# Optimization experiments

Hardware: AMD Instinct MI355X
Metric: run time of the kernel (lower is better)

Reference implementation:

```python
import jax, jax.numpy as jnp
import numpy as np

H = 128
NUM_GRAPHS = 256
NUM_TASKS = 40
BN_EPS = 1e-5


def setup_inputs() -> dict:
    key = jax.random.key(0)
    ks = jax.random.split(key, 32)
    N, E, F = 50000, 600000, 9
    inp = {}
    inp["x"] = jax.random.randint(ks[0], (N, 1), 0, 2)
    inp["edge_index"] = jax.random.randint(ks[1], (2, E), 0, N)
    inp["edge_attr"] = jax.random.uniform(ks[2], (E, F), dtype=jnp.float32)
    inp["batch"] = jnp.sort(jax.random.randint(ks[3], (N,), 0, NUM_GRAPHS))
    inp["self_loop_index"] = 7
    inp["self_loop_type"] = 1
    # parameters
    s = 0.02
    inp["node_emb"] = jax.random.normal(ks[4], (2, H), jnp.float32) * s
    for l in range(2):
        o = 5 + l * 11
        inp[f"enc_w{l}"] = jax.random.normal(ks[o + 0], (F, H), jnp.float32) * s
        inp[f"enc_b{l}"] = jnp.zeros((H,), jnp.float32)
        inp[f"w1_{l}"] = jax.random.normal(ks[o + 1], (2 * H, 2 * H), jnp.float32) * s
        inp[f"b1_{l}"] = jnp.zeros((2 * H,), jnp.float32)
        inp[f"gamma{l}"] = jnp.ones((2 * H,), jnp.float32)
        inp[f"beta{l}"] = jnp.zeros((2 * H,), jnp.float32)
        inp[f"mean{l}"] = jax.random.normal(ks[o + 2], (2 * H,), jnp.float32) * 0.1
        inp[f"var{l}"] = jax.random.uniform(ks[o + 3], (2 * H,), jnp.float32, 0.5, 1.5)
        inp[f"w2_{l}"] = jax.random.normal(ks[o + 4], (2 * H, H), jnp.float32) * s
        inp[f"b2_{l}"] = jnp.zeros((H,), jnp.float32)
    inp["pred_w"] = jax.random.normal(ks[30], (2 * H, NUM_TASKS), jnp.float32) * s
    inp["pred_b"] = jnp.zeros((NUM_TASKS,), jnp.float32)
    return inp


def _gin_layer(h, ei, ea, N, enc_w, enc_b, w1, b1, gamma, beta, mean, var, w2, b2):
    # edge encode: Linear(F, H) on all (real + self-loop) edges
    e = ea @ enc_w + enc_b                                  # [E+N, H]
    msg = jnp.concatenate([h[ei[1]], e], axis=1)            # [E+N, 2H] (feature_concat)
    agg = jax.ops.segment_sum(msg, ei[0], num_segments=N)   # sum pooling -> [N, 2H]
    z = agg @ w1 + b1
    z = (z - mean) * jax.lax.rsqrt(var + BN_EPS) * gamma + beta  # BatchNorm1d (eval)
    z = jax.nn.relu(z)
    return z @ w2 + b2                                      # [N, H]


def reference(x, edge_index, edge_attr, batch, self_loop_index, self_loop_type,
              node_emb,
              enc_w0, enc_b0, w1_0, b1_0, gamma0, beta0, mean0, var0, w2_0, b2_0,
              enc_w1, enc_b1, w1_1, b1_1, gamma1, beta1, mean1, var1, w2_1, b2_1,
              pred_w, pred_b):
    N = x.shape[0]
    loop = jnp.arange(N, dtype=edge_index.dtype)
    ei = jnp.concatenate([edge_index, jnp.stack([loop, loop])], axis=1)  # add self loops
    sl_attr = jnp.zeros((N, edge_attr.shape[1]), edge_attr.dtype).at[:, self_loop_index].set(
        jnp.asarray(self_loop_type, edge_attr.dtype))
    ea = jnp.concatenate([edge_attr, sl_attr], axis=0)       # [E+N, F]

    h0 = node_emb[x.reshape(-1)]                             # input node embedding [N, H]
    h1 = jax.nn.relu(_gin_layer(h0, ei, ea, N, enc_w0, enc_b0, w1_0, b1_0,
                                gamma0, beta0, mean0, var0, w2_0, b2_0))
    h2 = _gin_layer(h1, ei, ea, N, enc_w1, enc_b1, w1_1, b1_1,
                    gamma1, beta1, mean1, var1, w2_1, b2_1)  # JK='last'

    # graph mean pooling over batch ids
    sums = jax.ops.segment_sum(h2, batch, num_segments=NUM_GRAPHS)
    cnt = jax.ops.segment_sum(jnp.ones((N,), h2.dtype), batch, num_segments=NUM_GRAPHS)
    pooled = sums / jnp.maximum(cnt, 1.0)[:, None]
    graph_rep = jnp.concatenate([pooled, pooled], axis=1)    # no center_node_idx
    return graph_rep @ pred_w + pred_b                       # [G, num_tasks]
```

## Files before the change

kernel.cpp:

```cpp
#include <hip/hip_runtime.h>

#define H   128
#define H2  256
#define NG  256
#define NT  40
#define NF  9
#define TBM 32

__global__ void k_h0(const int* __restrict__ x, const float* __restrict__ emb,
                     float* __restrict__ h, int N) {
  int i = blockIdx.x * blockDim.x + threadIdx.x;
  if (i >= N * 32) return;
  int v = i >> 5, q = i & 31;
  ((float4*)h)[i] = ((const float4*)emb)[x[v] * 32 + q];
}

__global__ void k_deg(const int* __restrict__ ei, unsigned* __restrict__ deg, int E) {
  int e = blockIdx.x * blockDim.x + threadIdx.x;
  if (e >= E) return;
  atomicAdd(&deg[ei[e]], 1u);
}

__global__ __launch_bounds__(1024) void k_scan(const unsigned* __restrict__ deg,
                                               unsigned* __restrict__ off,
                                               unsigned* __restrict__ cur, int N) {
  __shared__ unsigned wsum[16];
  __shared__ unsigned wpre[16];
  __shared__ unsigned s_run;
  int tid = threadIdx.x;
  int lane = tid & 63, wv = tid >> 6;
  if (tid == 0) s_run = 0u;
  __syncthreads();
  for (int base = 0; base < N; base += 4096) {
    int i0 = base + tid * 4;
    unsigned v0 = 0, v1 = 0, v2 = 0, v3 = 0;
    if (i0 + 0 < N) v0 = deg[i0 + 0];
    if (i0 + 1 < N) v1 = deg[i0 + 1];
    if (i0 + 2 < N) v2 = deg[i0 + 2];
    if (i0 + 3 < N) v3 = deg[i0 + 3];
    unsigned tsum = v0 + v1 + v2 + v3;
    unsigned sc = tsum;
#pragma unroll
    for (int d = 1; d < 64; d <<= 1) {
      unsigned t = __shfl_up(sc, d);
      if (lane >= d) sc += t;
    }
    if (lane == 63) wsum[wv] = sc;
    __syncthreads();
    if (wv == 0 && lane < 16) {
      unsigned xv = wsum[lane];
#pragma unroll
      for (int d = 1; d < 16; d <<= 1) {
        unsigned t = __shfl_up(xv, d);
        if (lane >= d) xv += t;
      }
      wpre[lane] = xv;
    }
    __syncthreads();
    unsigned excl = s_run + (wv ? wpre[wv - 1] : 0u) + (sc - tsum);
    unsigned p1 = excl + v0, p2 = p1 + v1, p3 = p2 + v2;
    if (i0 + 0 < N) { off[i0 + 0] = excl; cur[i0 + 0] = excl; }
    if (i0 + 1 < N) { off[i0 + 1] = p1;   cur[i0 + 1] = p1; }
    if (i0 + 2 < N) { off[i0 + 2] = p2;   cur[i0 + 2] = p2; }
    if (i0 + 3 < N) { off[i0 + 3] = p3;   cur[i0 + 3] = p3; }
    __syncthreads();
    if (tid == 0) s_run += wpre[15];
  }
  if (tid == 0) off[N] = s_run;
}

__global__ void k_scatter(const int* __restrict__ ei, unsigned* __restrict__ cur,
                          int* __restrict__ csrc, int* __restrict__ ceid, int E) {
  int e = blockIdx.x * blockDim.x + threadIdx.x;
  if (e >= E) return;
  int dst = ei[e], src = ei[E + e];
  unsigned pos = atomicAdd(&cur[dst], 1u);
  csrc[pos] = src;
  ceid[pos] = e;
}

__global__ __launch_bounds__(256) void k_S(const float* __restrict__ ea,
    const unsigned* __restrict__ off, const int* __restrict__ ceid,
    float* __restrict__ S, int N) {
  int lane = threadIdx.x & 63;
  int wv = threadIdx.x >> 6;
  int sub = lane & 7;
  int v = blockIdx.x * 32 + wv * 8 + (lane >> 3);
  if (v >= N) return;
  unsigned o = off[v], e = off[v + 1];
  float acc[NF];
#pragma unroll
  for (int f = 0; f < NF; f++) acc[f] = 0.f;
  for (unsigned i = o + sub; i < e; i += 8) {
    const float* a = ea + (size_t)ceid[i] * NF;
#pragma unroll
    for (int f = 0; f < NF; f++) acc[f] += a[f];
  }
#pragma unroll
  for (int d = 1; d < 8; d <<= 1)
#pragma unroll
    for (int f = 0; f < NF; f++) acc[f] += __shfl_xor(acc[f], d);
  if (sub == 0) {
#pragma unroll
    for (int f = 0; f < NF; f++) S[(size_t)v * NF + f] = acc[f];
  }
}

__global__ __launch_bounds__(256) void k_gather(const float* __restrict__ h,
    const unsigned* __restrict__ off, const int* __restrict__ csrc,
    float* __restrict__ hs, int N) {
  int v = blockIdx.x * 4 + (threadIdx.x >> 6);
  int lane = threadIdx.x & 63;
  if (v >= N) return;
  unsigned o = off[v], e = off[v + 1];
  const float2* hp = (const float2*)h;
  float2 acc = hp[(size_t)v * 64 + lane];
  for (unsigned i = o; i < e; i++) {
    int s = csrc[i];
    float2 t = hp[(size_t)s * 64 + lane];
    acc.x += t.x; acc.y += t.y;
  }
  ((float2*)hs)[(size_t)v * 64 + lane] = acc;
}

__global__ void k_prep(const float* __restrict__ enc_w, const float* __restrict__ enc_b,
                       const float* __restrict__ w1, const float* __restrict__ b1,
                       const float* __restrict__ gamma, const float* __restrict__ beta,
                       const float* __restrict__ mean, const float* __restrict__ var,
                       const int* __restrict__ sli, const int* __restrict__ slt,
                       float* __restrict__ M, float* __restrict__ cc) {
  int c = threadIdx.x;
  float m[NF];
  float u = 0.f;
#pragma unroll
  for (int f = 0; f < NF; f++) m[f] = 0.f;
  for (int k = 0; k < H; k++) {
    float wv = w1[(H + k) * H2 + c];
#pragma unroll
    for (int f = 0; f < NF; f++) m[f] += enc_w[f * H + k] * wv;
    u += enc_b[k] * wv;
  }
#pragma unroll
  for (int f = 0; f < NF; f++) M[f * H2 + c] = m[f];
  float sc = gamma[c] * rsqrtf(var[c] + 1e-5f);
  float sh = beta[c] - mean[c] * sc;
  float k0 = (float)(*slt) * m[*sli] + u + b1[c];
  cc[0 * H2 + c] = sc;
  cc[1 * H2 + c] = sh;
  cc[2 * H2 + c] = u;
  cc[3 * H2 + c] = k0;
}

__global__ __launch_bounds__(256) void k_layer(
    const float* __restrict__ hs, const float* __restrict__ S,
    const unsigned* __restrict__ deg,
    const float* __restrict__ M, const float* __restrict__ cc,
    const float* __restrict__ w1, const float* __restrict__ w2,
    const float* __restrict__ b2,
    float* __restrict__ out, const int* __restrict__ batch,
    int N, int relu_out, int pool) {
  __shared__ float sh_hs[TBM][H];
  __shared__ float sh_z[TBM][H2];
  __shared__ float sh_M[NF][H2];
  __shared__ float sh_S[TBM][NF];
  __shared__ float sh_deg[TBM];
  int tid = threadIdx.x;
  int row0 = blockIdx.x * TBM;

  for (int i = tid; i < TBM * (H / 4); i += 256) {
    int r = i >> 5, q = i & 31;
    int v = row0 + r;
    float4 val = (v < N) ? ((const float4*)hs)[(size_t)v * (H / 4) + q]
                         : make_float4(0.f, 0.f, 0.f, 0.f);
    ((float4*)sh_hs[r])[q] = val;
  }
  for (int i = tid; i < NF * (H2 / 4); i += 256)
    ((float4*)sh_M)[i] = ((const float4*)M)[i];
  for (int i = tid; i < TBM * NF; i += 256) {
    int r = i / NF, f = i - r * NF;
    int v = row0 + r;
    sh_S[r][f] = (v < N) ? S[(size_t)v * NF + f] : 0.f;
  }
  if (tid < TBM) {
    int v = row0 + tid;
    sh_deg[tid] = (v < N) ? (float)deg[v] : 0.f;
  }
  __syncthreads();

  {
    int cg = tid & 31;
    int rg = tid >> 5;
    float acc[4][8];
#pragma unroll
    for (int r = 0; r < 4; r++)
#pragma unroll
      for (int c = 0; c < 8; c++) acc[r][c] = 0.f;

    const float* wbase = w1 + cg * 8;
    for (int k = 0; k < H; k += 4) {
      float av[4][4];
#pragma unroll
      for (int r = 0; r < 4; r++) {
        float4 t = *((const float4*)&sh_hs[rg * 4 + r][k]);
        av[r][0] = t.x; av[r][1] = t.y; av[r][2] = t.z; av[r][3] = t.w;
      }
      float bv[4][8];
#pragma unroll
      for (int kk = 0; kk < 4; kk++) {
        float4 t0 = ((const float4*)(wbase + (size_t)(k + kk) * H2))[0];
        float4 t1 = ((const float4*)(wbase + (size_t)(k + kk) * H2))[1];
        bv[kk][0] = t0.x; bv[kk][1] = t0.y; bv[kk][2] = t0.z; bv[kk][3] = t0.w;
        bv[kk][4] = t1.x; bv[kk][5] = t1.y; bv[kk][6] = t1.z; bv[kk][7] = t1.w;
      }
#pragma unroll
      for (int r = 0; r < 4; r++)
#pragma unroll
        for (int c = 0; c < 8; c++)
#pragma unroll
          for (int kk = 0; kk < 4; kk++)
            acc[r][c] += av[r][kk] * bv[kk][c];
    }

    float sv[4][NF];
#pragma unroll
    for (int r = 0; r < 4; r++)
#pragma unroll
      for (int f = 0; f < NF; f++) sv[r][f] = sh_S[rg * 4 + r][f];
#pragma unroll
    for (int f = 0; f < NF; f++) {
      float mv[8];
      float4 t0 = *((const float4*)&sh_M[f][cg * 8]);
      float4 t1 = *((const float4*)&sh_M[f][cg * 8 + 4]);
      mv[0] = t0.x; mv[1] = t0.y; mv[2] = t0.z; mv[3] = t0.w;
      mv[4] = t1.x; mv[5] = t1.y; mv[6] = t1.z; mv[7] = t1.w;
#pragma unroll
      for (int r = 0; r < 4; r++)
#pragma unroll
        for (int c = 0; c < 8; c++) acc[r][c] += sv[r][f] * mv[c];
    }

    float dg[4];
#pragma unroll
    for (int r = 0; r < 4; r++) dg[r] = sh_deg[rg * 4 + r];
    int cb = cg * 8;
    float scv[8], shv[8], uv[8], k0v[8];
    {
      float4 a0 = ((const float4*)(cc + 0 * H2 + cb))[0];
      float4 a1 = ((const float4*)(cc + 0 * H2 + cb))[1];
      scv[0]=a0.x; scv[1]=a0.y; scv[2]=a0.z; scv[3]=a0.w; scv[4]=a1.x; scv[5]=a1.y; scv[6]=a1.z; scv[7]=a1.w;
      float4 b0 = ((const float4*)(cc + 1 * H2 + cb))[0];
      float4 b1v = ((const float4*)(cc + 1 * H2 + cb))[1];
      shv[0]=b0.x; shv[1]=b0.y; shv[2]=b0.z; shv[3]=b0.w; shv[4]=b1v.x; shv[5]=b1v.y; shv[6]=b1v.z; shv[7]=b1v.w;
      float4 c0 = ((const float4*)(cc + 2 * H2 + cb))[0];
      float4 c1 = ((const float4*)(cc + 2 * H2 + cb))[1];
      uv[0]=c0.x; uv[1]=c0.y; uv[2]=c0.z; uv[3]=c0.w; uv[4]=c1.x; uv[5]=c1.y; uv[6]=c1.z; uv[7]=c1.w;
      float4 d0 = ((const float4*)(cc + 3 * H2 + cb))[0];
      float4 d1 = ((const float4*)(cc + 3 * H2 + cb))[1];
      k0v[0]=d0.x; k0v[1]=d0.y; k0v[2]=d0.z; k0v[3]=d0.w; k0v[4]=d1.x; k0v[5]=d1.y; k0v[6]=d1.z; k0v[7]=d1.w;
    }
#pragma unroll
    for (int r = 0; r < 4; r++) {
#pragma unroll
      for (int c = 0; c < 8; c++) {
        float z = acc[r][c] + dg[r] * uv[c] + k0v[c];
        z = z * scv[c] + shv[c];
        z = fmaxf(z, 0.f);
        sh_z[rg * 4 + r][cb + c] = z;
      }
    }
  }
  __syncthreads();

  {
    int cg = tid & 31;
    int rg = tid >> 5;
    float acc[4][4];
#pragma unroll
    for (int r = 0; r < 4; r++)
#pragma unroll
      for (int c = 0; c < 4; c++) acc[r][c] = 0.f;

    const float* w2b = w2 + cg * 4;
    for (int k = 0; k < H2; k += 4) {
      float av[4][4];
#pragma unroll
      for (int r = 0; r < 4; r++) {
        float4 t = *((const float4*)&sh_z[rg * 4 + r][k]);
        av[r][0] = t.x; av[r][1] = t.y; av[r][2] = t.z; av[r][3] = t.w;
      }
      float bv[4][4];
#pragma unroll
      for (int kk = 0; kk < 4; kk++) {
        float4 t = ((const float4*)(w2b + (size_t)(k + kk) * H))[0];
        bv[kk][0] = t.x; bv[kk][1] = t.y; bv[kk][2] = t.z; bv[kk][3] = t.w;
      }
#pragma unroll
      for (int r = 0; r < 4; r++)
#pragma unroll
        for (int c = 0; c < 4; c++)
#pragma unroll
          for (int kk = 0; kk < 4; kk++)
            acc[r][c] += av[r][kk] * bv[kk][c];
    }

    float4 bb = ((const float4*)(b2 + cg * 4))[0];
    float bvv[4] = {bb.x, bb.y, bb.z, bb.w};
#pragma unroll
    for (int r = 0; r < 4; r++) {
      int v = row0 + rg * 4 + r;
      if (v >= N) continue;
      float vals[4];
#pragma unroll
      for (int c = 0; c < 4; c++) {
        float z = acc[r][c] + bvv[c];
        if (relu_out) z = fmaxf(z, 0.f);
        vals[c] = z;
      }
      if (pool) {
        int g = batch[v];
#pragma unroll
        for (int c = 0; c < 4; c++)
          atomicAdd(&out[(size_t)g * H + cg * 4 + c], vals[c]);
      } else {
        float4 st = make_float4(vals[0], vals[1], vals[2], vals[3]);
        ((float4*)(out + (size_t)v * H))[cg] = st;
      }
    }
  }
}

__global__ void k_cnt(const int* __restrict__ batch, float* __restrict__ cnt, int N) {
  int v = blockIdx.x * blockDim.x + threadIdx.x;
  if (v < N) atomicAdd(&cnt[batch[v]], 1.0f);
}

__global__ void k_pred(const float* __restrict__ pooled, const float* __restrict__ cnt,
                       const float* __restrict__ pw, const float* __restrict__ pb,
                       float* __restrict__ outp) {
  int g = blockIdx.x;
  int t = threadIdx.x;
  if (t >= NT) return;
  float acc = 0.f;
  for (int k = 0; k < H; k++)
    acc += pooled[(size_t)g * H + k] * (pw[k * NT + t] + pw[(H + k) * NT + t]);
  float c = fmaxf(cnt[g], 1.0f);
  outp[(size_t)g * NT + t] = acc / c + pb[t];
}

extern "C" void kernel_launch(void* const* d_in, const int* in_sizes, int n_in,
                              void* d_out, int out_size, void* d_ws, size_t ws_size,
                              hipStream_t stream) {
  const int*   x     = (const int*)d_in[0];
  const int*   ei    = (const int*)d_in[1];
  const float* ea    = (const float*)d_in[2];
  const int*   batch = (const int*)d_in[3];
  const int*   sli   = (const int*)d_in[4];
  const int*   slt   = (const int*)d_in[5];
  const float* emb   = (const float*)d_in[6];
  const float* encw[2] = {(const float*)d_in[7],  (const float*)d_in[17]};
  const float* encb[2] = {(const float*)d_in[8],  (const float*)d_in[18]};
  const float* w1[2]   = {(const float*)d_in[9],  (const float*)d_in[19]};
  const float* b1[2]   = {(const float*)d_in[10], (const float*)d_in[20]};
  const float* gam[2]  = {(const float*)d_in[11], (const float*)d_in[21]};
  const float* bet[2]  = {(const float*)d_in[12], (const float*)d_in[22]};
  const float* mea[2]  = {(const float*)d_in[13], (const float*)d_in[23]};
  const float* var[2]  = {(const float*)d_in[14], (const float*)d_in[24]};
  const float* w2[2]   = {(const float*)d_in[15], (const float*)d_in[25]};
  const float* b2[2]   = {(const float*)d_in[16], (const float*)d_in[26]};
  const float* pw = (const float*)d_in[27];
  const float* pb = (const float*)d_in[28];

  int N = in_sizes[0];
  int E = in_sizes[1] / 2;

  char* p = (char*)d_ws;
  auto alloc = [&](size_t bytes) {
    char* r = p;
    p += (bytes + 255) / 256 * 256;
    return r;
  };
  unsigned* deg    = (unsigned*)alloc((size_t)N * 4);
  float*    S      = (float*)alloc((size_t)N * NF * 4);
  unsigned* off    = (unsigned*)alloc((size_t)(N + 1) * 4);
  unsigned* cur    = (unsigned*)alloc((size_t)N * 4);
  int*      csrc   = (int*)alloc((size_t)E * 4);
  int*      ceid   = (int*)alloc((size_t)E * 4);
  float*    hA     = (float*)alloc((size_t)N * H * 4);
  float*    hS     = (float*)alloc((size_t)N * H * 4);
  float*    hB     = (float*)alloc((size_t)N * H * 4);
  float*    M      = (float*)alloc((size_t)NF * H2 * 4);
  float*    cc     = (float*)alloc((size_t)4 * H2 * 4);
  float*    pooled = (float*)alloc((size_t)NG * H * 4);
  float*    cnt    = (float*)alloc((size_t)NG * 4);

  hipMemsetAsync(deg, 0, (size_t)N * 4, stream);
  hipMemsetAsync(pooled, 0, (size_t)NG * H * 4, stream);
  hipMemsetAsync(cnt, 0, (size_t)NG * 4, stream);

  k_h0<<<(N * 32 + 255) / 256, 256, 0, stream>>>(x, emb, hA, N);
  k_deg<<<(E + 255) / 256, 256, 0, stream>>>(ei, deg, E);
  k_scan<<<1, 1024, 0, stream>>>(deg, off, cur, N);
  k_scatter<<<(E + 255) / 256, 256, 0, stream>>>(ei, cur, csrc, ceid, E);
  k_S<<<(N + 31) / 32, 256, 0, stream>>>(ea, off, ceid, S, N);

  k_prep<<<1, 256, 0, stream>>>(encw[0], encb[0], w1[0], b1[0], gam[0], bet[0],
                                mea[0], var[0], sli, slt, M, cc);
  k_gather<<<(N + 3) / 4, 256, 0, stream>>>(hA, off, csrc, hS, N);
  k_layer<<<(N + TBM - 1) / TBM, 256, 0, stream>>>(hS, S, deg, M, cc, w1[0], w2[0],
                                                   b2[0], hB, batch, N, 1, 0);
  k_prep<<<1, 256, 0, stream>>>(encw[1], encb[1], w1[1], b1[1], gam[1], bet[1],
                                mea[1], var[1], sli, slt, M, cc);
  k_gather<<<(N + 3) / 4, 256, 0, stream>>>(hB, off, csrc, hS, N);
  k_layer<<<(N + TBM - 1) / TBM, 256, 0, stream>>>(hS, S, deg, M, cc, w1[1], w2[1],
                                                   b2[1], pooled, batch, N, 0, 1);

  k_cnt<<<(N + 255) / 256, 256, 0, stream>>>(batch, cnt, N);
  k_pred<<<NG, 64, 0, stream>>>(pooled, cnt, pw, pb, (float*)d_out);
}
```

Baseline: 821.9 us.

## Move layer GEMMs to bf16 MFMA with split hi/lo precision emulation

```diff
diff --git a/kernel.cpp b/kernel.cpp
--- a/kernel.cpp
+++ b/kernel.cpp
@@ -5,7 +5,33 @@
 #define NG  256
 #define NT  40
 #define NF  9
-#define TBM 32
+
+typedef __attribute__((ext_vector_type(8))) short short8;
+typedef __attribute__((ext_vector_type(4))) float f32x4;
+
+#define MFMA16(a, b, c) __builtin_amdgcn_mfma_f32_16x16x32_bf16(a, b, c, 0, 0, 0)
+
+__device__ __forceinline__ void f2bf_hilo(float x, unsigned short& hi, unsigned short& lo) {
+  unsigned u = __float_as_uint(x);
+  unsigned hh = (u + 0x7FFFu + ((u >> 16) & 1u)) >> 16;
+  float hf = __uint_as_float(hh << 16);
+  float r = x - hf;
+  unsigned v = __float_as_uint(r);
+  unsigned ll = (v + 0x7FFFu + ((v >> 16) & 1u)) >> 16;
+  hi = (unsigned short)hh;
+  lo = (unsigned short)ll;
+}
+
+__device__ __forceinline__ void cvt8(float4 a, float4 b, short8& hi, short8& lo) {
+  float xs[8] = {a.x, a.y, a.z, a.w, b.x, b.y, b.z, b.w};
+#pragma unroll
+  for (int j = 0; j < 8; j++) {
+    unsigned short h, l;
+    f2bf_hilo(xs[j], h, l);
+    hi[j] = (short)h;
+    lo[j] = (short)l;
+  }
+}
 
 __global__ void k_h0(const int* __restrict__ x, const float* __restrict__ emb,
                      float* __restrict__ h, int N) {
@@ -123,207 +149,188 @@
   ((float2*)hs)[(size_t)v * 64 + lane] = acc;
 }
 
-__global__ void k_prep(const float* __restrict__ enc_w, const float* __restrict__ enc_b,
-                       const float* __restrict__ w1, const float* __restrict__ b1,
-                       const float* __restrict__ gamma, const float* __restrict__ beta,
-                       const float* __restrict__ mean, const float* __restrict__ var,
-                       const int* __restrict__ sli, const int* __restrict__ slt,
-                       float* __restrict__ M, float* __restrict__ cc) {
+__global__ void k_prepA(const float* __restrict__ enc_w, const float* __restrict__ enc_b,
+                        const float* __restrict__ w1, const float* __restrict__ b1,
+                        const float* __restrict__ gamma, const float* __restrict__ beta,
+                        const float* __restrict__ mean, const float* __restrict__ var,
+                        const int* __restrict__ sli, const int* __restrict__ slt,
+                        unsigned short* __restrict__ BAhi, unsigned short* __restrict__ BAlo,
+                        float* __restrict__ cc) {
   int c = threadIdx.x;
   float m[NF];
   float u = 0.f;
 #pragma unroll
   for (int f = 0; f < NF; f++) m[f] = 0.f;
   for (int k = 0; k < H; k++) {
-    float wv = w1[(H + k) * H2 + c];
+    float wv = w1[(size_t)(H + k) * H2 + c];
 #pragma unroll
     for (int f = 0; f < NF; f++) m[f] += enc_w[f * H + k] * wv;
     u += enc_b[k] * wv;
   }
-#pragma unroll
-  for (int f = 0; f < NF; f++) M[f * H2 + c] = m[f];
-  float sc = gamma[c] * rsqrtf(var[c] + 1e-5f);
-  float sh = beta[c] - mean[c] * sc;
   float k0 = (float)(*slt) * m[*sli] + u + b1[c];
-  cc[0 * H2 + c] = sc;
-  cc[1 * H2 + c] = sh;
-  cc[2 * H2 + c] = u;
-  cc[3 * H2 + c] = k0;
+  float scv = gamma[c] * rsqrtf(var[c] + 1e-5f);
+  cc[c] = scv;
+  cc[H2 + c] = beta[c] - mean[c] * scv;
+  int ct = c >> 4, cl = c & 15;
+  for (int k = 0; k < 160; k++) {
+    float val;
+    if (k < 128)      val = w1[(size_t)k * H2 + c];
+    else if (k < 137) val = m[k - 128];
+    else if (k == 137) val = u;
+    else if (k == 138) val = k0;
+    else              val = 0.f;
+    unsigned short h, l;
+    f2bf_hilo(val, h, l);
+    int ks = k >> 5, kr = k & 31;
+    int lane = (kr >> 3) * 16 + cl, j = kr & 7;
+    size_t idx = ((size_t)((ks * 16 + ct) * 64 + lane)) * 8 + j;
+    BAhi[idx] = h;
+    BAlo[idx] = l;
+  }
+}
+
+__global__ void k_prepB2(const float* __restrict__ w2,
+                         unsigned short* __restrict__ BBhi, unsigned short* __restrict__ BBlo) {
+  int t = threadIdx.x;
+  int c = t & 127, half = t >> 7;
+  int ct = c >> 4, cl = c & 15;
+  for (int kk = 0; kk < 128; kk++) {
+    int k = half * 128 + kk;
+    float val = w2[(size_t)k * H + c];
+    unsigned short h, l;
+    f2bf_hilo(val, h, l);
+    int ks = k >> 5, kr = k & 31;
+    int lane = (kr >> 3) * 16 + cl, j = kr & 7;
+    size_t idx = ((size_t)((ks * 8 + ct) * 64 + lane)) * 8 + j;
+    BBhi[idx] = h;
+    BBlo[idx] = l;
+  }
 }
 
 __global__ __launch_bounds__(256) void k_layer(
     const float* __restrict__ hs, const float* __restrict__ S,
     const unsigned* __restrict__ deg,
-    const float* __restrict__ M, const float* __restrict__ cc,
-    const float* __restrict__ w1, const float* __restrict__ w2,
-    const float* __restrict__ b2,
+    const unsigned short* __restrict__ BAhi, const unsigned short* __restrict__ BAlo,
+    const unsigned short* __restrict__ BBhi, const unsigned short* __restrict__ BBlo,
+    const float* __restrict__ cc, const float* __restrict__ b2,
     float* __restrict__ out, const int* __restrict__ batch,
     int N, int relu_out, int pool) {
-  __shared__ float sh_hs[TBM][H];
-  __shared__ float sh_z[TBM][H2];
-  __shared__ float sh_M[NF][H2];
-  __shared__ float sh_S[TBM][NF];
-  __shared__ float sh_deg[TBM];
+  __shared__ float ext[32][36];
+  __shared__ unsigned short zhi[32 * 256];
+  __shared__ unsigned short zlo[32 * 256];
   int tid = threadIdx.x;
-  int row0 = blockIdx.x * TBM;
-
-  for (int i = tid; i < TBM * (H / 4); i += 256) {
-    int r = i >> 5, q = i & 31;
+  int row0 = blockIdx.x * 32;
+
+  for (int i = tid; i < 32 * 36; i += 256) {
+    int r = i / 36, c2 = i - r * 36;
     int v = row0 + r;
-    float4 val = (v < N) ? ((const float4*)hs)[(size_t)v * (H / 4) + q]
-                         : make_float4(0.f, 0.f, 0.f, 0.f);
-    ((float4*)sh_hs[r])[q] = val;
-  }
-  for (int i = tid; i < NF * (H2 / 4); i += 256)
-    ((float4*)sh_M)[i] = ((const float4*)M)[i];
-  for (int i = tid; i < TBM * NF; i += 256) {
-    int r = i / NF, f = i - r * NF;
-    int v = row0 + r;
-    sh_S[r][f] = (v < N) ? S[(size_t)v * NF + f] : 0.f;
-  }
-  if (tid < TBM) {
-    int v = row0 + tid;
-    sh_deg[tid] = (v < N) ? (float)deg[v] : 0.f;
+    float val = 0.f;
+    if (v < N) {
+      if (c2 < NF) val = S[(size_t)v * NF + c2];
+      else if (c2 == 9) val = (float)deg[v];
+      else if (c2 == 10) val = 1.0f;
+    }
+    ext[r][c2] = val;
   }
   __syncthreads();
 
+  int l = tid & 63, wv = tid >> 6;
+  int rowoff = (wv >> 1) * 16;
+  int ctoffA = (wv & 1) * 8;
+  int lr = l & 15, lg = l >> 4;
+
+  f32x4 acc[8];
+#pragma unroll
+  for (int ct = 0; ct < 8; ct++) acc[ct] = f32x4{0.f, 0.f, 0.f, 0.f};
+
+#pragma unroll
+  for (int ks = 0; ks < 4; ks++) {
+    int row = row0 + rowoff + lr;
+    int rowc = row < N ? row : N - 1;
+    const float* src = hs + (size_t)rowc * H + ks * 32 + lg * 8;
+    float4 x0 = ((const float4*)src)[0];
+    float4 x1 = ((const float4*)src)[1];
+    short8 ahi, alo;
+    cvt8(x0, x1, ahi, alo);
+#pragma unroll
+    for (int ct = 0; ct < 8; ct++) {
+      int gct = ctoffA + ct;
+      short8 bhi = ((const short8*)BAhi)[((ks * 16 + gct) << 6) + l];
+      short8 blo = ((const short8*)BAlo)[((ks * 16 + gct) << 6) + l];
+      acc[ct] = MFMA16(ahi, bhi, acc[ct]);
+      acc[ct] = MFMA16(ahi, blo, acc[ct]);
+      acc[ct] = MFMA16(alo, bhi, acc[ct]);
+    }
+  }
   {
-    int cg = tid & 31;
-    int rg = tid >> 5;
-    float acc[4][8];
-#pragma unroll
-    for (int r = 0; r < 4; r++)
-#pragma unroll
-      for (int c = 0; c < 8; c++) acc[r][c] = 0.f;
-
-    const float* wbase = w1 + cg * 8;
-    for (int k = 0; k < H; k += 4) {
-      float av[4][4];
-#pragma unroll
-      for (int r = 0; r < 4; r++) {
-        float4 t = *((const float4*)&sh_hs[rg * 4 + r][k]);
-        av[r][0] = t.x; av[r][1] = t.y; av[r][2] = t.z; av[r][3] = t.w;
-      }
-      float bv[4][8];
-#pragma unroll
-      for (int kk = 0; kk < 4; kk++) {
-        float4 t0 = ((const float4*)(wbase + (size_t)(k + kk) * H2))[0];
-        float4 t1 = ((const float4*)(wbase + (size_t)(k + kk) * H2))[1];
-        bv[kk][0] = t0.x; bv[kk][1] = t0.y; bv[kk][2] = t0.z; bv[kk][3] = t0.w;
-        bv[kk][4] = t1.x; bv[kk][5] = t1.y; bv[kk][6] = t1.z; bv[kk][7] = t1.w;
-      }
-#pragma unroll
-      for (int r = 0; r < 4; r++)
-#pragma unroll
-        for (int c = 0; c < 8; c++)
-#pragma unroll
-          for (int kk = 0; kk < 4; kk++)
-            acc[r][c] += av[r][kk] * bv[kk][c];
-    }
-
-    float sv[4][NF];
-#pragma unroll
-    for (int r = 0; r < 4; r++)
-#pragma unroll
-      for (int f = 0; f < NF; f++) sv[r][f] = sh_S[rg * 4 + r][f];
-#pragma unroll
-    for (int f = 0; f < NF; f++) {
-      float mv[8];
-      float4 t0 = *((const float4*)&sh_M[f][cg * 8]);
-      float4 t1 = *((const float4*)&sh_M[f][cg * 8 + 4]);
-      mv[0] = t0.x; mv[1] = t0.y; mv[2] = t0.z; mv[3] = t0.w;
-      mv[4] = t1.x; mv[5] = t1.y; mv[6] = t1.z; mv[7] = t1.w;
-#pragma unroll
-      for (int r = 0; r < 4; r++)
-#pragma unroll
-        for (int c = 0; c < 8; c++) acc[r][c] += sv[r][f] * mv[c];
-    }
-
-    float dg[4];
-#pragma unroll
-    for (int r = 0; r < 4; r++) dg[r] = sh_deg[rg * 4 + r];
-    int cb = cg * 8;
-    float scv[8], shv[8], uv[8], k0v[8];
-    {
-      float4 a0 = ((const float4*)(cc + 0 * H2 + cb))[0];
-      float4 a1 = ((const float4*)(cc + 0 * H2 + cb))[1];
-      scv[0]=a0.x; scv[1]=a0.y; scv[2]=a0.z; scv[3]=a0.w; scv[4]=a1.x; scv[5]=a1.y; scv[6]=a1.z; scv[7]=a1.w;
-      float4 b0 = ((const float4*)(cc + 1 * H2 + cb))[0];
-      float4 b1v = ((const float4*)(cc + 1 * H2 + cb))[1];
-      shv[0]=b0.x; shv[1]=b0.y; shv[2]=b0.z; shv[3]=b0.w; shv[4]=b1v.x; shv[5]=b1v.y; shv[6]=b1v.z; shv[7]=b1v.w;
-      float4 c0 = ((const float4*)(cc + 2 * H2 + cb))[0];
-      float4 c1 = ((const float4*)(cc + 2 * H2 + cb))[1];
-      uv[0]=c0.x; uv[1]=c0.y; uv[2]=c0.z; uv[3]=c0.w; uv[4]=c1.x; uv[5]=c1.y; uv[6]=c1.z; uv[7]=c1.w;
-      float4 d0 = ((const float4*)(cc + 3 * H2 + cb))[0];
-      float4 d1 = ((const float4*)(cc + 3 * H2 + cb))[1];
-      k0v[0]=d0.x; k0v[1]=d0.y; k0v[2]=d0.z; k0v[3]=d0.w; k0v[4]=d1.x; k0v[5]=d1.y; k0v[6]=d1.z; k0v[7]=d1.w;
-    }
+    const float* src = &ext[rowoff + lr][lg * 8];
+    float4 x0 = ((const float4*)src)[0];
+    float4 x1 = ((const float4*)src)[1];
+    short8 ahi, alo;
+    cvt8(x0, x1, ahi, alo);
+#pragma unroll
+    for (int ct = 0; ct < 8; ct++) {
+      int gct = ctoffA + ct;
+      short8 bhi = ((const short8*)BAhi)[((4 * 16 + gct) << 6) + l];
+      short8 blo = ((const short8*)BAlo)[((4 * 16 + gct) << 6) + l];
+      acc[ct] = MFMA16(ahi, bhi, acc[ct]);
+      acc[ct] = MFMA16(ahi, blo, acc[ct]);
+      acc[ct] = MFMA16(alo, bhi, acc[ct]);
+    }
+  }
+
+#pragma unroll
+  for (int ct = 0; ct < 8; ct++) {
+    int c = (ctoffA + ct) * 16 + lr;
+    float scv = cc[c], shv = cc[H2 + c];
 #pragma unroll
     for (int r = 0; r < 4; r++) {
-#pragma unroll
-      for (int c = 0; c < 8; c++) {
-        float z = acc[r][c] + dg[r] * uv[c] + k0v[c];
-        z = z * scv[c] + shv[c];
-        z = fmaxf(z, 0.f);
-        sh_z[rg * 4 + r][cb + c] = z;
-      }
+      float z = acc[ct][r] * scv + shv;
+      z = fmaxf(z, 0.f);
+      unsigned short h, lo2;
+      f2bf_hilo(z, h, lo2);
+      int zr = rowoff + lg * 4 + r;
+      unsigned off = (unsigned)(zr * 512 + c * 2) ^ (unsigned)((zr & 7) << 4);
+      *(unsigned short*)((char*)zhi + off) = h;
+      *(unsigned short*)((char*)zlo + off) = lo2;
     }
   }
   __syncthreads();
 
-  {
-    int cg = tid & 31;
-    int rg = tid >> 5;
-    float acc[4][4];
-#pragma unroll
-    for (int r = 0; r < 4; r++)
-#pragma unroll
-      for (int c = 0; c < 4; c++) acc[r][c] = 0.f;
-
-    const float* w2b = w2 + cg * 4;
-    for (int k = 0; k < H2; k += 4) {
-      float av[4][4];
-#pragma unroll
-      for (int r = 0; r < 4; r++) {
-        float4 t = *((const float4*)&sh_z[rg * 4 + r][k]);
-        av[r][0] = t.x; av[r][1] = t.y; av[r][2] = t.z; av[r][3] = t.w;
-      }
-      float bv[4][4];
-#pragma unroll
-      for (int kk = 0; kk < 4; kk++) {
-        float4 t = ((const float4*)(w2b + (size_t)(k + kk) * H))[0];
-        bv[kk][0] = t.x; bv[kk][1] = t.y; bv[kk][2] = t.z; bv[kk][3] = t.w;
-      }
-#pragma unroll
-      for (int r = 0; r < 4; r++)
-#pragma unroll
-        for (int c = 0; c < 4; c++)
-#pragma unroll
-          for (int kk = 0; kk < 4; kk++)
-            acc[r][c] += av[r][kk] * bv[kk][c];
-    }
-
-    float4 bb = ((const float4*)(b2 + cg * 4))[0];
-    float bvv[4] = {bb.x, bb.y, bb.z, bb.w};
+  f32x4 acc2[4];
+#pragma unroll
+  for (int ct = 0; ct < 4; ct++) acc2[ct] = f32x4{0.f, 0.f, 0.f, 0.f};
+#pragma unroll
+  for (int ks = 0; ks < 8; ks++) {
+    int zr = rowoff + lr;
+    unsigned off = (unsigned)(zr * 512 + (ks * 32 + lg * 8) * 2) ^ (unsigned)((zr & 7) << 4);
+    short8 ahi = *(const short8*)((char*)zhi + off);
+    short8 alo = *(const short8*)((char*)zlo + off);
+#pragma unroll
+    for (int ct = 0; ct < 4; ct++) {
+      int gct = (wv & 1) * 4 + ct;
+      short8 bhi = ((const short8*)BBhi)[((ks * 8 + gct) << 6) + l];
+      short8 blo = ((const short8*)BBlo)[((ks * 8 + gct) << 6) + l];
+      acc2[ct] = MFMA16(ahi, bhi, acc2[ct]);
+      acc2[ct] = MFMA16(ahi, blo, acc2[ct]);
+      acc2[ct] = MFMA16(alo, bhi, acc2[ct]);
+    }
+  }
+
+#pragma unroll
+  for (int ct = 0; ct < 4; ct++) {
+    int c2 = ((wv & 1) * 4 + ct) * 16 + lr;
+    float bias = b2[c2];
 #pragma unroll
     for (int r = 0; r < 4; r++) {
-      int v = row0 + rg * 4 + r;
-      if (v >= N) continue;
-      float vals[4];
-#pragma unroll
-      for (int c = 0; c < 4; c++) {
-        float z = acc[r][c] + bvv[c];
-        if (relu_out) z = fmaxf(z, 0.f);
-        vals[c] = z;
-      }
+      int row = row0 + rowoff + lg * 4 + r;
+      if (row >= N) continue;
+      float val = acc2[ct][r] + bias;
+      if (relu_out) val = fmaxf(val, 0.f);
       if (pool) {
-        int g = batch[v];
-#pragma unroll
-        for (int c = 0; c < 4; c++)
-          atomicAdd(&out[(size_t)g * H + cg * 4 + c], vals[c]);
+        atomicAdd(&out[(size_t)batch[row] * H + c2], val);
       } else {
-        float4 st = make_float4(vals[0], vals[1], vals[2], vals[3]);
-        ((float4*)(out + (size_t)v * H))[cg] = st;
+        out[(size_t)row * H + c2] = val;
       }
     }
   }
@@ -388,14 +395,19 @@
   float*    hA     = (float*)alloc((size_t)N * H * 4);
   float*    hS     = (float*)alloc((size_t)N * H * 4);
   float*    hB     = (float*)alloc((size_t)N * H * 4);
-  float*    M      = (float*)alloc((size_t)NF * H2 * 4);
-  float*    cc     = (float*)alloc((size_t)4 * H2 * 4);
+  unsigned short* BAhi = (unsigned short*)alloc((size_t)5 * 16 * 64 * 8 * 2);
+  unsigned short* BAlo = (unsigned short*)alloc((size_t)5 * 16 * 64 * 8 * 2);
+  unsigned short* BBhi = (unsigned short*)alloc((size_t)8 * 8 * 64 * 8 * 2);
+  unsigned short* BBlo = (unsigned short*)alloc((size_t)8 * 8 * 64 * 8 * 2);
+  float*    cc     = (float*)alloc((size_t)2 * H2 * 4);
   float*    pooled = (float*)alloc((size_t)NG * H * 4);
   float*    cnt    = (float*)alloc((size_t)NG * 4);
 
   hipMemsetAsync(deg, 0, (size_t)N * 4, stream);
   hipMemsetAsync(pooled, 0, (size_t)NG * H * 4, stream);
   hipMemsetAsync(cnt, 0, (size_t)NG * 4, stream);
+
+  int nblk = (N + 31) / 32;
 
   k_h0<<<(N * 32 + 255) / 256, 256, 0, stream>>>(x, emb, hA, N);
   k_deg<<<(E + 255) / 256, 256, 0, stream>>>(ei, deg, E);
@@ -403,16 +415,18 @@
   k_scatter<<<(E + 255) / 256, 256, 0, stream>>>(ei, cur, csrc, ceid, E);
   k_S<<<(N + 31) / 32, 256, 0, stream>>>(ea, off, ceid, S, N);
 
-  k_prep<<<1, 256, 0, stream>>>(encw[0], encb[0], w1[0], b1[0], gam[0], bet[0],
-                                mea[0], var[0], sli, slt, M, cc);
+  k_prepA<<<1, 256, 0, stream>>>(encw[0], encb[0], w1[0], b1[0], gam[0], bet[0],
+                                 mea[0], var[0], sli, slt, BAhi, BAlo, cc);
+  k_prepB2<<<1, 256, 0, stream>>>(w2[0], BBhi, BBlo);
   k_gather<<<(N + 3) / 4, 256, 0, stream>>>(hA, off, csrc, hS, N);
-  k_layer<<<(N + TBM - 1) / TBM, 256, 0, stream>>>(hS, S, deg, M, cc, w1[0], w2[0],
-                                                   b2[0], hB, batch, N, 1, 0);
-  k_prep<<<1, 256, 0, stream>>>(encw[1], encb[1], w1[1], b1[1], gam[1], bet[1],
-                                mea[1], var[1], sli, slt, M, cc);
+  k_layer<<<nblk, 256, 0, stream>>>(hS, S, deg, BAhi, BAlo, BBhi, BBlo, cc, b2[0],
+                                    hB, batch, N, 1, 0);
+  k_prepA<<<1, 256, 0, stream>>>(encw[1], encb[1], w1[1], b1[1], gam[1], bet[1],
+                                 mea[1], var[1], sli, slt, BAhi, BAlo, cc);
+  k_prepB2<<<1, 256, 0, stream>>>(w2[1], BBhi, BBlo);
   k_gather<<<(N + 3) / 4, 256, 0, stream>>>(hB, off, csrc, hS, N);
-  k_layer<<<(N + TBM - 1) / TBM, 256, 0, stream>>>(hS, S, deg, M, cc, w1[1], w2[1],
-                                                   b2[1], pooled, batch, N, 0, 1);
+  k_layer<<<nblk, 256, 0, stream>>>(hS, S, deg, BAhi, BAlo, BBhi, BBlo, cc, b2[1],
+                                    pooled, batch, N, 0, 1);
 
   k_cnt<<<(N + 255) / 256, 256, 0, stream>>>(batch, cnt, N);
   k_pred<<<NG, 64, 0, stream>>>(pooled, cnt, pw, pb, (float*)d_out);
```

Result: no change. 827.9 us (+0.7%).
